# Optimization experiments

Measured on AMD Instinct MI355X. Metric: run time of the kernel, lower is better.

The kernel has to match this reference:

```python
import jax, jax.numpy as jnp
import numpy as np

N, E, F_IN, H, C, G, NCLS = 50000, 400000, 128, 8, 64, 64, 10
NEG_SLOPE = 0.2
EPS = 1e-16


def gat_conv(x, W, att_src, att_dst, bias, src, dst, concat):
    n = x.shape[0]
    h = (x @ W).reshape(n, H, C)                      # [N,H,C]
    a_src = jnp.sum(h * att_src, axis=-1)             # [N,H]
    a_dst = jnp.sum(h * att_dst, axis=-1)             # [N,H]
    alpha = jax.nn.leaky_relu(a_src[src] + a_dst[dst], NEG_SLOPE)  # [E,H]
    # segment softmax over incoming edges of each destination node
    amax = jax.ops.segment_max(alpha, dst, num_segments=n)
    ex = jnp.exp(alpha - amax[dst])
    denom = jax.ops.segment_sum(ex, dst, num_segments=n)
    alpha = ex / (denom[dst] + EPS)
    msg = h[src] * alpha[:, :, None]                  # [E,H,C]
    out = jax.ops.segment_sum(msg, dst, num_segments=n)  # [N,H,C]
    out = out.reshape(n, H * C) if concat else out.mean(axis=1)
    return out + bias


def setup_inputs() -> dict:
    key = jax.random.key(0)
    ks = jax.random.split(key, 20)
    x = jax.random.normal(ks[0], (N, F_IN), dtype=jnp.float32)
    edge_index = jax.random.randint(ks[1], (2, E), 0, N, dtype=jnp.int32)
    batch = jnp.sort(jax.random.randint(ks[2], (N,), 0, G, dtype=jnp.int32))
    def glorot(k, shape):
        fan = sum(shape[-2:]) if len(shape) >= 2 else shape[-1]
        return jax.random.normal(k, shape, dtype=jnp.float32) * jnp.sqrt(2.0 / fan)
    return {
        "x": x, "edge_index": edge_index, "batch": batch,
        "W1": glorot(ks[3], (F_IN, H * C)),
        "a1s": glorot(ks[4], (H, C)), "a1d": glorot(ks[5], (H, C)),
        "b1": jnp.zeros((H * C,), jnp.float32),
        "W2": glorot(ks[6], (H * C, H * C)),
        "a2s": glorot(ks[7], (H, C)), "a2d": glorot(ks[8], (H, C)),
        "b2": jnp.zeros((H * C,), jnp.float32),
        "W3": glorot(ks[9], (H * C, H * C)),
        "a3s": glorot(ks[10], (H, C)), "a3d": glorot(ks[11], (H, C)),
        "b3": jnp.zeros((C,), jnp.float32),
        "fcw": glorot(ks[12], (C, NCLS)),
        "fcb": jnp.zeros((NCLS,), jnp.float32),
    }


def reference(x, edge_index, batch, W1, a1s, a1d, b1, W2, a2s, a2d, b2,
              W3, a3s, a3d, b3, fcw, fcb):
    n = x.shape[0]
    # PyG GATConv default add_self_loops=True
    loops = jnp.arange(n, dtype=edge_index.dtype)
    src = jnp.concatenate([edge_index[0], loops])
    dst = jnp.concatenate([edge_index[1], loops])

    h = jax.nn.relu(gat_conv(x, W1, a1s, a1d, b1, src, dst, True))
    h = jax.nn.relu(gat_conv(h, W2, a2s, a2d, b2, src, dst, True))
    h = jax.nn.relu(gat_conv(h, W3, a3s, a3d, b3, src, dst, False))  # [N,C]

    # global mean pool over graphs
    sums = jax.ops.segment_sum(h, batch, num_segments=G)
    cnts = jax.ops.segment_sum(jnp.ones((n, 1), h.dtype), batch, num_segments=G)
    pooled = sums / jnp.maximum(cnts, 1.0)            # [G,C]

    return jax.nn.log_softmax(pooled @ fcw + fcb, axis=-1)
```

## Files before the change

kernel.cpp:

```cpp
#include <hip/hip_runtime.h>
#include <hip/hip_bf16.h>

#define HH 8
#define CC 64
#define HC 512
#define GG 64
#define NCLS 10
#define F_IN 128
#define NEG_SLOPE 0.2f
#define EPS_ 1e-16f
#define MAXD 32

typedef float f32x4 __attribute__((ext_vector_type(4)));
typedef __bf16 bf16x8 __attribute__((ext_vector_type(8)));

__device__ __forceinline__ unsigned short f2bf(float f) {
    unsigned u = __builtin_bit_cast(unsigned, f);
    u += 0x7fffu + ((u >> 16) & 1u);
    return (unsigned short)(u >> 16);
}
__device__ __forceinline__ float bflo(unsigned u) {
    return __builtin_bit_cast(float, u << 16);
}
__device__ __forceinline__ float bfhi(unsigned u) {
    return __builtin_bit_cast(float, u & 0xffff0000u);
}
__device__ __forceinline__ unsigned char f2fp8(float f) {
    unsigned pk = __builtin_amdgcn_cvt_pk_fp8_f32(f, f, 0u, false);
    return (unsigned char)(pk & 0xffu);
}
template <int SEL>
__device__ __forceinline__ float fp82f(unsigned w) {
    return __builtin_amdgcn_cvt_f32_fp8(w, SEL);
}
#define ACC_FP8(hv, w)                                           \
    acc[0] += (w) * fp82f<0>(hv.x); acc[1] += (w) * fp82f<1>(hv.x); \
    acc[2] += (w) * fp82f<2>(hv.x); acc[3] += (w) * fp82f<3>(hv.x); \
    acc[4] += (w) * fp82f<0>(hv.y); acc[5] += (w) * fp82f<1>(hv.y); \
    acc[6] += (w) * fp82f<2>(hv.y); acc[7] += (w) * fp82f<3>(hv.y);

__device__ __forceinline__ void gload16(const unsigned short* g, unsigned short* l) {
    __builtin_amdgcn_global_load_lds(
        (const __attribute__((address_space(1))) unsigned int*)g,
        (__attribute__((address_space(3))) unsigned int*)l,
        16, 0, 0);
}

__global__ void hist_kernel(const int* __restrict__ ei, int* __restrict__ counts,
                            int E_, int EP_) {
    int e = blockIdx.x * 256 + threadIdx.x;
    if (e >= EP_) return;
    int d = (e < E_) ? ei[E_ + e] : (e - E_);
    atomicAdd(&counts[d], 1);
}

__global__ void scan1(const int* __restrict__ counts, int* __restrict__ partial,
                      int* __restrict__ bsum, int n) {
    __shared__ int buf[256];
    int idx = blockIdx.x * 256 + threadIdx.x;
    int v = (idx < n) ? counts[idx] : 0;
    buf[threadIdx.x] = v;
    __syncthreads();
    for (int off = 1; off < 256; off <<= 1) {
        int t = (threadIdx.x >= off) ? buf[threadIdx.x - off] : 0;
        __syncthreads();
        buf[threadIdx.x] += t;
        __syncthreads();
    }
    if (idx < n) partial[idx] = buf[threadIdx.x];
    if (threadIdx.x == 255) bsum[blockIdx.x] = buf[255];
}

__global__ void scan2(int* __restrict__ bsum, int nb) {
    __shared__ int buf[1024];
    int t = threadIdx.x;
    buf[t] = (t < nb) ? bsum[t] : 0;
    __syncthreads();
    for (int off = 1; off < 1024; off <<= 1) {
        int v = (t >= off) ? buf[t - off] : 0;
        __syncthreads();
        buf[t] += v;
        __syncthreads();
    }
    if (t < nb) bsum[t] = buf[t];
}

__global__ void scan3(const int* __restrict__ partial, const int* __restrict__ bsum,
                      int* __restrict__ row_start, int* __restrict__ counts, int n) {
    int idx = blockIdx.x * 256 + threadIdx.x;
    if (idx >= n) return;
    int add = (blockIdx.x > 0) ? bsum[blockIdx.x - 1] : 0;
    row_start[idx + 1] = partial[idx] + add;
    counts[idx] = 0;
    if (idx == 0) row_start[0] = 0;
}

__global__ void scatter_kernel(const int* __restrict__ ei, const int* __restrict__ row_start,
                               int* __restrict__ cursor, int* __restrict__ src_sorted,
                               int E_, int EP_) {
    int e = blockIdx.x * 256 + threadIdx.x;
    if (e >= EP_) return;
    int s, d;
    if (e < E_) { s = ei[e]; d = ei[E_ + e]; }
    else        { s = e - E_; d = e - E_; }
    int pos = row_start[d] + atomicAdd(&cursor[d], 1);
    src_sorted[pos] = s;
}

__global__ void conv_bf16(const float* __restrict__ in, unsigned short* __restrict__ out,
                          int n4) {
    int i = blockIdx.x * 256 + threadIdx.x;
    if (i >= n4) return;
    float4 v = reinterpret_cast<const float4*>(in)[i];
    reinterpret_cast<ushort4*>(out)[i] =
        make_ushort4(f2bf(v.x), f2bf(v.y), f2bf(v.z), f2bf(v.w));
}

__global__ void transpose_w(const float* __restrict__ W, unsigned short* __restrict__ WT,
                            int K, int Nc) {
    __shared__ float t[32][33];
    int bx = blockIdx.x * 32;
    int by = blockIdx.y * 32;
    int x = threadIdx.x, y = threadIdx.y;
    for (int i = y; i < 32; i += 8)
        t[i][x] = W[(size_t)(by + i) * Nc + bx + x];
    __syncthreads();
    for (int i = y; i < 32; i += 8)
        WT[(size_t)(bx + i) * K + by + x] = f2bf(t[x][i]);
}

__global__ void make_wsd(const float* __restrict__ W, const float* __restrict__ as_,
                         const float* __restrict__ ad_, unsigned short* __restrict__ BX,
                         int K) {
    int k = blockIdx.x;
    int lane = threadIdx.x & 63;
    int head = lane >> 3;
    int coff = (lane & 7) * 8;
    const float* wr = W + (size_t)k * HC + head * 64 + coff;
    const float* asp = as_ + head * 64 + coff;
    const float* adp = ad_ + head * 64 + coff;
    float ps = 0.f, pd = 0.f;
#pragma unroll
    for (int i = 0; i < 8; ++i) {
        float wv = wr[i];
        ps += wv * asp[i];
        pd += wv * adp[i];
    }
    ps += __shfl_xor(ps, 1); pd += __shfl_xor(pd, 1);
    ps += __shfl_xor(ps, 2); pd += __shfl_xor(pd, 2);
    ps += __shfl_xor(ps, 4); pd += __shfl_xor(pd, 4);
    if ((lane & 7) == 0) {
        BX[(size_t)head * K + k] = f2bf(ps);
        BX[(size_t)(8 + head) * K + k] = f2bf(pd);
    }
}

__global__ __launch_bounds__(256) void gemm_attn(const unsigned short* __restrict__ A,
                                                 const unsigned short* __restrict__ BT,
                                                 const unsigned short* __restrict__ BX,
                                                 unsigned char* __restrict__ C,
                                                 float* __restrict__ a_src,
                                                 float* __restrict__ a_dst,
                                                 int M, int K) {
    __shared__ __align__(16) unsigned short As[128 * 64];
    __shared__ __align__(16) unsigned short Bs[128 * 64];
    __shared__ __align__(16) unsigned short Bxs[16 * 64];

    const int nwg = gridDim.x;
    const int f = blockIdx.x;
    const int q = nwg >> 3, r = nwg & 7;
    const int xcd = f & 7, rank = f >> 3;
    const int swz = (xcd < r ? xcd * (q + 1) : r * (q + 1) + (xcd - r) * q) + rank;
    const int bcol = (swz & 3) * 128;
    const int brow = (swz >> 2) * 128;

    const int tid = threadIdx.x;
    const int lane = tid & 63;
    const int wave = tid >> 6;
    const int wr = wave >> 1, wc = wave & 1;
    const bool do_x = (wc == 0) && (bcol == 0);

    f32x4 acc[4][4];
#pragma unroll
    for (int i = 0; i < 4; ++i)
#pragma unroll
        for (int j = 0; j < 4; ++j) acc[i][j] = (f32x4)0.f;
    f32x4 accx[4];
#pragma unroll
    for (int i = 0; i < 4; ++i) accx[i] = (f32x4)0.f;

    const int lrow = lane >> 3;
    const int lcolsw = (((lane & 7) ^ lrow)) * 8;
    const int arow0 = brow + wave * 32 + lrow;
    const int brow0 = bcol + wave * 32 + lrow;

    const int kb = (lane >> 4) * 8;
    const int rowa = wr * 64 + (lane & 15);
    const int rowb = wc * 64 + (lane & 15);
    const int rxor = lane & 7;

    for (int k0 = 0; k0 < K; k0 += 64) {
#pragma unroll
        for (int it = 0; it < 4; ++it) {
            const int c = wave * 4 + it;
            int ar = arow0 + it * 8;
            if (ar >= M) ar = M - 1;
            gload16(A + (size_t)ar * K + k0 + lcolsw, &As[c * 512]);
            int br = brow0 + it * 8;
            gload16(BT + (size_t)br * K + k0 + lcolsw, &Bs[c * 512]);
        }
        if (bcol == 0 && wave < 2)
            gload16(BX + (size_t)(wave * 8 + lrow) * K + k0 + lcolsw, &Bxs[wave * 512]);
        __syncthreads();
#pragma unroll
        for (int kk = 0; kk < 64; kk += 32) {
            const int chunk = (kk + kb) >> 3;
            const int koff = (chunk ^ rxor) * 8;
            bf16x8 a[4], b[4];
#pragma unroll
            for (int m = 0; m < 4; ++m)
                a[m] = *(const bf16x8*)&As[(rowa + m * 16) * 64 + koff];
#pragma unroll
            for (int nn = 0; nn < 4; ++nn)
                b[nn] = *(const bf16x8*)&Bs[(rowb + nn * 16) * 64 + koff];
#pragma unroll
            for (int m = 0; m < 4; ++m)
#pragma unroll
                for (int nn = 0; nn < 4; ++nn)
                    acc[m][nn] = __builtin_amdgcn_mfma_f32_16x16x32_bf16(
                        a[m], b[nn], acc[m][nn], 0, 0, 0);
            if (do_x) {
                bf16x8 bx = *(const bf16x8*)&Bxs[(lane & 15) * 64 + koff];
#pragma unroll
                for (int m = 0; m < 4; ++m)
                    accx[m] = __builtin_amdgcn_mfma_f32_16x16x32_bf16(
                        a[m], bx, accx[m], 0, 0, 0);
            }
        }
        __syncthreads();
    }

    const int r0 = brow + wr * 64 + (lane >> 4) * 4;
    const int c0 = bcol + wc * 64 + (lane & 15);

#pragma unroll
    for (int m = 0; m < 4; ++m)
#pragma unroll
        for (int j = 0; j < 4; ++j) {
            int rr = r0 + m * 16 + j;
            if (rr < M) {
#pragma unroll
                for (int nn = 0; nn < 4; ++nn)
                    C[(size_t)rr * HC + c0 + nn * 16] = f2fp8(acc[m][nn][j]);
            }
        }

    if (do_x) {
        const int col16 = lane & 15;
        float* dst = (col16 < 8) ? a_src : a_dst;
        const int head = col16 & 7;
#pragma unroll
        for (int m = 0; m < 4; ++m)
#pragma unroll
            for (int j = 0; j < 4; ++j) {
                int rr = r0 + m * 16 + j;
                if (rr < M) dst[rr * 8 + head] = accx[m][j];
            }
    }
}

template <int MODE>
__global__ __launch_bounds__(256) void agg_kernel(const unsigned char* __restrict__ h,
                                                  const float* __restrict__ a_src,
                                                  const float* __restrict__ a_dst,
                                                  const float* __restrict__ bias,
                                                  const int* __restrict__ row_start,
                                                  const int* __restrict__ src_sorted,
                                                  void* __restrict__ outv, int n) {
    __shared__ float alds[4][MAXD][8];
    __shared__ int   slds[4][MAXD];
    int ws = threadIdx.x >> 6;
    int d = blockIdx.x * 4 + ws;
    int lane = threadIdx.x & 63;
    if (d >= n) return;
    int base = row_start[d];
    int end = row_start[d + 1];
    int deg = end - base;
    int head = lane & 7;
    int eslot = lane >> 3;
    float adh = a_dst[d * 8 + head];

    float mx = -1e30f;
    for (int idx = eslot; idx < deg; idx += 8) {
        int s = src_sorted[base + idx];
        float al = a_src[s * 8 + head] + adh;
        al = (al > 0.f) ? al : NEG_SLOPE * al;
        if (idx < MAXD) {
            alds[ws][idx][head] = al;
            if (head == 0) slds[ws][idx] = s;
        }
        mx = fmaxf(mx, al);
    }
    mx = fmaxf(mx, __shfl_xor(mx, 8));
    mx = fmaxf(mx, __shfl_xor(mx, 16));
    mx = fmaxf(mx, __shfl_xor(mx, 32));

    float sm = 0.f;
    for (int idx = eslot; idx < deg; idx += 8) {
        float e;
        if (idx < MAXD) {
            float al = alds[ws][idx][head];
            e = __expf(al - mx);
            alds[ws][idx][head] = e;
        } else {
            int s = src_sorted[base + idx];
            float al = a_src[s * 8 + head] + adh;
            al = (al > 0.f) ? al : NEG_SLOPE * al;
            e = __expf(al - mx);
        }
        sm += e;
    }
    sm += __shfl_xor(sm, 8);
    sm += __shfl_xor(sm, 16);
    sm += __shfl_xor(sm, 32);
    float inv = 1.0f / (sm + EPS_);

    asm volatile("s_waitcnt lgkmcnt(0)" ::: "memory");
    __builtin_amdgcn_wave_barrier();

    int hd2 = lane >> 3;
    float mx2 = __shfl(mx, hd2);
    float inv2 = __shfl(inv, hd2);
    float adh2 = a_dst[d * 8 + hd2];
    const unsigned char* hl = h + lane * 8;

    float acc[8] = {};
    int mdeg = (deg < MAXD) ? deg : MAXD;
    for (int i = 0; i < mdeg; i += 4) {
        int i0 = i;
        int i1 = (i + 1 < mdeg) ? i + 1 : mdeg - 1;
        int i2 = (i + 2 < mdeg) ? i + 2 : mdeg - 1;
        int i3 = (i + 3 < mdeg) ? i + 3 : mdeg - 1;
        int s0 = slds[ws][i0], s1 = slds[ws][i1];
        int s2 = slds[ws][i2], s3 = slds[ws][i3];
        uint2 h0 = *reinterpret_cast<const uint2*>(hl + (size_t)s0 * HC);
        uint2 h1 = *reinterpret_cast<const uint2*>(hl + (size_t)s1 * HC);
        uint2 h2 = *reinterpret_cast<const uint2*>(hl + (size_t)s2 * HC);
        uint2 h3 = *reinterpret_cast<const uint2*>(hl + (size_t)s3 * HC);
        float w0 = alds[ws][i0][hd2] * inv2;
        float w1 = (i + 1 < mdeg) ? alds[ws][i1][hd2] * inv2 : 0.f;
        float w2 = (i + 2 < mdeg) ? alds[ws][i2][hd2] * inv2 : 0.f;
        float w3 = (i + 3 < mdeg) ? alds[ws][i3][hd2] * inv2 : 0.f;
        ACC_FP8(h0, w0)
        ACC_FP8(h1, w1)
        ACC_FP8(h2, w2)
        ACC_FP8(h3, w3)
    }
    for (int i = base + MAXD; i < end; ++i) {
        int s = src_sorted[i];
        float al = a_src[s * 8 + hd2] + adh2;
        al = (al > 0.f) ? al : NEG_SLOPE * al;
        float w = __expf(al - mx2) * inv2;
        uint2 hv = *reinterpret_cast<const uint2*>(hl + (size_t)s * HC);
        ACC_FP8(hv, w)
    }

    if (MODE == 0) {
        float4 b0 = *reinterpret_cast<const float4*>(bias + lane * 8);
        float4 b1 = *reinterpret_cast<const float4*>(bias + lane * 8 + 4);
        float v[8];
        v[0] = fmaxf(acc[0] + b0.x, 0.f); v[1] = fmaxf(acc[1] + b0.y, 0.f);
        v[2] = fmaxf(acc[2] + b0.z, 0.f); v[3] = fmaxf(acc[3] + b0.w, 0.f);
        v[4] = fmaxf(acc[4] + b1.x, 0.f); v[5] = fmaxf(acc[5] + b1.y, 0.f);
        v[6] = fmaxf(acc[6] + b1.z, 0.f); v[7] = fmaxf(acc[7] + b1.w, 0.f);
        uint4 o;
        o.x = (unsigned)f2bf(v[0]) | ((unsigned)f2bf(v[1]) << 16);
        o.y = (unsigned)f2bf(v[2]) | ((unsigned)f2bf(v[3]) << 16);
        o.z = (unsigned)f2bf(v[4]) | ((unsigned)f2bf(v[5]) << 16);
        o.w = (unsigned)f2bf(v[6]) | ((unsigned)f2bf(v[7]) << 16);
        *reinterpret_cast<uint4*>((unsigned short*)outv + (size_t)d * HC + lane * 8) = o;
    } else {
#pragma unroll
        for (int j = 0; j < 8; ++j) {
            acc[j] += __shfl_xor(acc[j], 8);
            acc[j] += __shfl_xor(acc[j], 16);
            acc[j] += __shfl_xor(acc[j], 32);
        }
        if (lane < 8) {
            float* op = (float*)outv + (size_t)d * 64 + lane * 8;
            float4 o0, o1;
            o0.x = fmaxf(acc[0] * 0.125f + bias[lane * 8 + 0], 0.f);
            o0.y = fmaxf(acc[1] * 0.125f + bias[lane * 8 + 1], 0.f);
            o0.z = fmaxf(acc[2] * 0.125f + bias[lane * 8 + 2], 0.f);
            o0.w = fmaxf(acc[3] * 0.125f + bias[lane * 8 + 3], 0.f);
            o1.x = fmaxf(acc[4] * 0.125f + bias[lane * 8 + 4], 0.f);
            o1.y = fmaxf(acc[5] * 0.125f + bias[lane * 8 + 5], 0.f);
            o1.z = fmaxf(acc[6] * 0.125f + bias[lane * 8 + 6], 0.f);
            o1.w = fmaxf(acc[7] * 0.125f + bias[lane * 8 + 7], 0.f);
            *reinterpret_cast<float4*>(op) = o0;
            *reinterpret_cast<float4*>(op + 4) = o1;
        }
    }
}

__global__ __launch_bounds__(256) void pool_partial(const float* __restrict__ h3,
                                                    const int* __restrict__ batch,
                                                    float* __restrict__ pooled,
                                                    int* __restrict__ cnt, int n) {
    int g = blockIdx.x >> 3;
    int part = blockIdx.x & 7;
    __shared__ int s_lo, s_hi;
    if (threadIdx.x == 0) {
        int lo = 0, hi = n;
        while (lo < hi) { int mid = (lo + hi) >> 1; if (batch[mid] < g) lo = mid + 1; else hi = mid; }
        s_lo = lo;
        int lo2 = lo, hi2 = n;
        while (lo2 < hi2) { int mid = (lo2 + hi2) >> 1; if (batch[mid] < g + 1) lo2 = mid + 1; else hi2 = mid; }
        s_hi = lo2;
    }
    __syncthreads();
    int lo = s_lo, hi = s_hi;
    int len = hi - lo;
    if (part == 0 && threadIdx.x == 0) cnt[g] = len;
    int start = lo + (part * len) / 8;
    int stop  = lo + ((part + 1) * len) / 8;
    int lane = threadIdx.x & 63;
    int slot = threadIdx.x >> 6;
    float acc = 0.f;
    for (int i = start + slot; i < stop; i += 4)
        acc += h3[(size_t)i * 64 + lane];
    __shared__ float red[4][64];
    red[slot][lane] = acc;
    __syncthreads();
    if (slot == 0) {
        float v = red[0][lane] + red[1][lane] + red[2][lane] + red[3][lane];
        atomicAdd(&pooled[g * 64 + lane], v);
    }
}

__global__ void classify_kernel(const float* __restrict__ pooled,
                                const int* __restrict__ cnt,
                                const float* __restrict__ fcw,
                                const float* __restrict__ fcb,
                                float* __restrict__ out) {
    int g = blockIdx.x;
    int lane = threadIdx.x & 63;
    float c = (float)cnt[g];
    c = fmaxf(c, 1.0f);
    float p = pooled[g * 64 + lane] / c;
    float logit[NCLS];
#pragma unroll
    for (int j = 0; j < NCLS; ++j) {
        float t = p * fcw[lane * NCLS + j];
#pragma unroll
        for (int off = 1; off < 64; off <<= 1) t += __shfl_xor(t, off);
        logit[j] = t + fcb[j];
    }
    float m = logit[0];
#pragma unroll
    for (int j = 1; j < NCLS; ++j) m = fmaxf(m, logit[j]);
    float s = 0.f;
#pragma unroll
    for (int j = 0; j < NCLS; ++j) s += expf(logit[j] - m);
    float lse = logf(s);
    if (lane < NCLS) {
        float v = logit[0];
#pragma unroll
        for (int j = 1; j < NCLS; ++j)
            if (lane == j) v = logit[j];
        out[g * NCLS + lane] = v - m - lse;
    }
}

extern "C" void kernel_launch(void* const* d_in, const int* in_sizes, int n_in,
                              void* d_out, int out_size, void* d_ws, size_t ws_size,
                              hipStream_t stream) {
    const float* x    = (const float*)d_in[0];
    const int*   ei   = (const int*)d_in[1];
    const int*   batch = (const int*)d_in[2];
    const float* W1  = (const float*)d_in[3];
    const float* a1s = (const float*)d_in[4];
    const float* a1d = (const float*)d_in[5];
    const float* b1  = (const float*)d_in[6];
    const float* W2  = (const float*)d_in[7];
    const float* a2s = (const float*)d_in[8];
    const float* a2d = (const float*)d_in[9];
    const float* b2  = (const float*)d_in[10];
    const float* W3  = (const float*)d_in[11];
    const float* a3s = (const float*)d_in[12];
    const float* a3d = (const float*)d_in[13];
    const float* b3  = (const float*)d_in[14];
    const float* fcw = (const float*)d_in[15];
    const float* fcb = (const float*)d_in[16];

    const int n  = in_sizes[0] / F_IN;
    const int E_ = in_sizes[1] / 2;
    const int EP = E_ + n;

    char* p = (char*)d_ws;
    unsigned short* xb   = (unsigned short*)p; p += (size_t)n * F_IN * 2;
    unsigned short* w1t  = (unsigned short*)p; p += (size_t)HC * F_IN * 2;
    unsigned short* w2t  = (unsigned short*)p; p += (size_t)HC * HC * 2;
    unsigned short* w3t  = (unsigned short*)p; p += (size_t)HC * HC * 2;
    unsigned short* bx1  = (unsigned short*)p; p += (size_t)16 * F_IN * 2;
    unsigned short* bx2  = (unsigned short*)p; p += (size_t)16 * HC * 2;
    unsigned short* bx3  = (unsigned short*)p; p += (size_t)16 * HC * 2;
    unsigned char*  hbuf = (unsigned char*)p;  p += (size_t)n * HC;
    unsigned short* buf2 = (unsigned short*)p; p += (size_t)n * HC * 2;
    float* asrc   = (float*)p; p += (size_t)n * 8 * 4;
    float* adst   = (float*)p; p += (size_t)n * 8 * 4;
    float* h3     = (float*)p; p += (size_t)n * 64 * 4;
    float* pooled = (float*)p; p += (size_t)GG * 64 * 4;
    int* cnt      = (int*)p;   p += (size_t)GG * 4;
    int* counts   = (int*)p;   p += (size_t)n * 4;
    int* row_start= (int*)p;   p += (size_t)(n + 1) * 4;
    int* src_sorted=(int*)p;   p += (size_t)EP * 4;
    int* partial  = (int*)p;   p += (size_t)n * 4;
    int* bsum     = (int*)p;   p += 1024 * 4;

    const int edge_blocks = (EP + 255) / 256;
    const int node_blocks = (n + 3) / 4;
    const int scan_blocks = (n + 255) / 256;

    hipMemsetAsync(counts, 0, (size_t)n * sizeof(int), stream);
    hist_kernel<<<edge_blocks, 256, 0, stream>>>(ei, counts, E_, EP);
    scan1<<<scan_blocks, 256, 0, stream>>>(counts, partial, bsum, n);
    scan2<<<1, 1024, 0, stream>>>(bsum, scan_blocks);
    scan3<<<scan_blocks, 256, 0, stream>>>(partial, bsum, row_start, counts, n);
    scatter_kernel<<<edge_blocks, 256, 0, stream>>>(ei, row_start, counts, src_sorted, E_, EP);

    conv_bf16<<<((n * F_IN / 4) + 255) / 256, 256, 0, stream>>>(x, xb, n * F_IN / 4);
    transpose_w<<<dim3(HC / 32, F_IN / 32), dim3(32, 8), 0, stream>>>(W1, w1t, F_IN, HC);
    transpose_w<<<dim3(HC / 32, HC / 32), dim3(32, 8), 0, stream>>>(W2, w2t, HC, HC);
    transpose_w<<<dim3(HC / 32, HC / 32), dim3(32, 8), 0, stream>>>(W3, w3t, HC, HC);
    make_wsd<<<F_IN, 64, 0, stream>>>(W1, a1s, a1d, bx1, F_IN);
    make_wsd<<<HC, 64, 0, stream>>>(W2, a2s, a2d, bx2, HC);
    make_wsd<<<HC, 64, 0, stream>>>(W3, a3s, a3d, bx3, HC);

    const int nby = (n + 127) / 128;
    const int nwg = 4 * nby;

    gemm_attn<<<nwg, 256, 0, stream>>>(xb, w1t, bx1, hbuf, asrc, adst, n, F_IN);
    agg_kernel<0><<<node_blocks, 256, 0, stream>>>(hbuf, asrc, adst, b1, row_start, src_sorted, buf2, n);

    gemm_attn<<<nwg, 256, 0, stream>>>(buf2, w2t, bx2, hbuf, asrc, adst, n, HC);
    agg_kernel<0><<<node_blocks, 256, 0, stream>>>(hbuf, asrc, adst, b2, row_start, src_sorted, buf2, n);

    gemm_attn<<<nwg, 256, 0, stream>>>(buf2, w3t, bx3, hbuf, asrc, adst, n, HC);
    agg_kernel<1><<<node_blocks, 256, 0, stream>>>(hbuf, asrc, adst, b3, row_start, src_sorted, h3, n);

    hipMemsetAsync(pooled, 0, (size_t)(GG * 64) * sizeof(float), stream);
    pool_partial<<<GG * 8, 256, 0, stream>>>(h3, batch, pooled, cnt, n);
    classify_kernel<<<GG, 64, 0, stream>>>(pooled, cnt, fcw, fcb, (float*)d_out);
}
```

Measured before the change: 350.9 us.

## Double-buffer LDS tiles in gemm_attn with K-step of 32

Restructures the GEMM main loop to use two LDS buffers with a K-tile of 32 and a new swizzle pattern. The next tile's global-to-LDS loads are issued before computing on the current tile, and one barrier per iteration replaces two. The aim is to overlap memory loads with MFMA compute. The tradeoff is twice as many loop iterations with less MFMA work per barrier, and correctness depends on the async load timing relative to the single barrier.

```diff
diff --git a/kernel.cpp b/kernel.cpp
--- a/kernel.cpp
+++ b/kernel.cpp
@@ -162,9 +162,9 @@
                                                  float* __restrict__ a_src,
                                                  float* __restrict__ a_dst,
                                                  int M, int K) {
-    __shared__ __align__(16) unsigned short As[128 * 64];
-    __shared__ __align__(16) unsigned short Bs[128 * 64];
-    __shared__ __align__(16) unsigned short Bxs[16 * 64];
+    __shared__ __align__(16) unsigned short As[2 * 128 * 32];
+    __shared__ __align__(16) unsigned short Bs[2 * 128 * 32];
+    __shared__ __align__(16) unsigned short Bxs[2 * 16 * 32];
 
     const int nwg = gridDim.x;
     const int f = blockIdx.x;
@@ -178,7 +178,8 @@
     const int lane = tid & 63;
     const int wave = tid >> 6;
     const int wr = wave >> 1, wc = wave & 1;
-    const bool do_x = (wc == 0) && (bcol == 0);
+    const bool do_bx = (bcol == 0);
+    const bool do_x = (wc == 0) && do_bx;
 
     f32x4 acc[4][4];
 #pragma unroll
@@ -189,53 +190,61 @@
 #pragma unroll
     for (int i = 0; i < 4; ++i) accx[i] = (f32x4)0.f;
 
-    const int lrow = lane >> 3;
-    const int lcolsw = (((lane & 7) ^ lrow)) * 8;
-    const int arow0 = brow + wave * 32 + lrow;
-    const int brow0 = bcol + wave * 32 + lrow;
-
-    const int kb = (lane >> 4) * 8;
+    const int lrow4 = lane >> 2;
+    const int srcoff = (((lane & 3) ^ ((lrow4 >> 1) & 3))) * 8;
+    const int arow_b = brow + wave * 16 + lrow4;
+    const int brow_b = bcol + wave * 16 + lrow4;
+
+    const int koff = (((lane >> 4) ^ ((lane >> 1) & 3))) * 8;
     const int rowa = wr * 64 + (lane & 15);
     const int rowb = wc * 64 + (lane & 15);
-    const int rxor = lane & 7;
-
-    for (int k0 = 0; k0 < K; k0 += 64) {
-#pragma unroll
-        for (int it = 0; it < 4; ++it) {
-            const int c = wave * 4 + it;
-            int ar = arow0 + it * 8;
+
+    const int nt = K >> 5;
+
+    auto STAGE = [&](int buf, int t) {
+        const int k0 = t * 32;
+#pragma unroll
+        for (int round = 0; round < 2; ++round) {
+            int ar = arow_b + round * 64;
             if (ar >= M) ar = M - 1;
-            gload16(A + (size_t)ar * K + k0 + lcolsw, &As[c * 512]);
-            int br = brow0 + it * 8;
-            gload16(BT + (size_t)br * K + k0 + lcolsw, &Bs[c * 512]);
-        }
-        if (bcol == 0 && wave < 2)
-            gload16(BX + (size_t)(wave * 8 + lrow) * K + k0 + lcolsw, &Bxs[wave * 512]);
-        __syncthreads();
-#pragma unroll
-        for (int kk = 0; kk < 64; kk += 32) {
-            const int chunk = (kk + kb) >> 3;
-            const int koff = (chunk ^ rxor) * 8;
-            bf16x8 a[4], b[4];
+            gload16(A + (size_t)ar * K + k0 + srcoff,
+                    &As[buf * 4096 + (round * 64 + wave * 16) * 32]);
+            int br = brow_b + round * 64;
+            gload16(BT + (size_t)br * K + k0 + srcoff,
+                    &Bs[buf * 4096 + (round * 64 + wave * 16) * 32]);
+        }
+        if (do_bx && wave == 0)
+            gload16(BX + (size_t)lrow4 * K + k0 + srcoff, &Bxs[buf * 512]);
+    };
+
+    STAGE(0, 0);
+    __syncthreads();
+
+    for (int t = 0; t < nt; ++t) {
+        const int cur = t & 1;
+        if (t + 1 < nt) STAGE(cur ^ 1, t + 1);
+
+        const unsigned short* Ab = &As[cur * 4096];
+        const unsigned short* Bb = &Bs[cur * 4096];
+        bf16x8 a[4], b[4];
+#pragma unroll
+        for (int m = 0; m < 4; ++m)
+            a[m] = *(const bf16x8*)&Ab[(rowa + m * 16) * 32 + koff];
+#pragma unroll
+        for (int nn = 0; nn < 4; ++nn)
+            b[nn] = *(const bf16x8*)&Bb[(rowb + nn * 16) * 32 + koff];
+#pragma unroll
+        for (int m = 0; m < 4; ++m)
+#pragma unroll
+            for (int nn = 0; nn < 4; ++nn)
+                acc[m][nn] = __builtin_amdgcn_mfma_f32_16x16x32_bf16(
+                    a[m], b[nn], acc[m][nn], 0, 0, 0);
+        if (do_x) {
+            bf16x8 bx = *(const bf16x8*)&Bxs[cur * 512 + (lane & 15) * 32 + koff];
 #pragma unroll
             for (int m = 0; m < 4; ++m)
-                a[m] = *(const bf16x8*)&As[(rowa + m * 16) * 64 + koff];
-#pragma unroll
-            for (int nn = 0; nn < 4; ++nn)
-                b[nn] = *(const bf16x8*)&Bs[(rowb + nn * 16) * 64 + koff];
-#pragma unroll
-            for (int m = 0; m < 4; ++m)
-#pragma unroll
-                for (int nn = 0; nn < 4; ++nn)
-                    acc[m][nn] = __builtin_amdgcn_mfma_f32_16x16x32_bf16(
-                        a[m], b[nn], acc[m][nn], 0, 0, 0);
-            if (do_x) {
-                bf16x8 bx = *(const bf16x8*)&Bxs[(lane & 15) * 64 + koff];
-#pragma unroll
-                for (int m = 0; m < 4; ++m)
-                    accx[m] = __builtin_amdgcn_mfma_f32_16x16x32_bf16(
-                        a[m], bx, accx[m], 0, 0, 0);
-            }
+                accx[m] = __builtin_amdgcn_mfma_f32_16x16x32_bf16(
+                    a[m], bx, accx[m], 0, 0, 0);
         }
         __syncthreads();
     }
```

Result: no change. 354.4 us (+1.0%).
